# Kernel tuning notes

Hardware: AMD Instinct MI355X
Metric: run time of the kernel (lower is better)

The kernel has to match this reference:

```python
import jax, jax.numpy as jnp
import numpy as np
from jax import lax


def _maxpool_nchw(x, k):
    # Non-overlapping kxk max pool over the last two dims (NCHW).
    return lax.reduce_window(x, -jnp.inf, lax.max,
                             window_dimensions=(1, 1, k, k),
                             window_strides=(1, 1, k, k),
                             padding='VALID')


def setup_inputs() -> dict:
    key = jax.random.key(0)
    k1, k2, k3, k4, k5 = jax.random.split(key, 5)
    B = 16
    return {
        'input_tensor1': jax.random.normal(k1, (B, 128, 48, 48), jnp.float32),
        'input_tensor2': jax.random.normal(k2, (B, 64, 96, 96), jnp.float32),
        'input_tensor3': jax.random.normal(k3, (B, 32, 192, 192), jnp.float32),
        'input_tensor4': jax.random.normal(k4, (B, 16, 384, 384), jnp.float32),
        'pure_ff': jax.random.normal(k5, (B, 256, 24, 24), jnp.float32),
    }


def reference(input_tensor1, input_tensor2, input_tensor3, input_tensor4, pure_ff):
    # and then max-pools. Pooling is per-channel, so this equals pooling once
    # and tiling the pooled result along the channel axis -- same math,
    # without materializing the redundant concat intermediates.
    x1 = jnp.tile(_maxpool_nchw(input_tensor1, 2), (1, 2, 1, 1))   # [B,256,24,24]
    x2 = jnp.tile(_maxpool_nchw(input_tensor2, 4), (1, 4, 1, 1))   # [B,256,24,24]
    x3 = jnp.tile(_maxpool_nchw(input_tensor3, 8), (1, 8, 1, 1))   # [B,256,24,24]
    x4 = jnp.tile(_maxpool_nchw(input_tensor4, 16), (1, 16, 1, 1)) # [B,256,24,24]
    return jax.nn.relu(x1 + x2 + x3 + x4 + pure_ff)
```

## Files before the change

kernel.cpp:

```cpp
#include <hip/hip_runtime.h>
#include <math.h>


namespace {

constexpr int OHW = 24;

__device__ __forceinline__ float fmax4(const float4 v) {
  return fmaxf(fmaxf(v.x, v.y), fmaxf(v.z, v.w));
}

__global__ __launch_bounds__(256, 3) void fused_block(const float* __restrict__ x1,
                                                      const float* __restrict__ x2,
                                                      const float* __restrict__ x3,
                                                      const float* __restrict__ x4,
                                                      const float* __restrict__ ff,
                                                      float* __restrict__ out) {
  __shared__ __attribute__((aligned(16))) float s1[128 * 12];
  __shared__ __attribute__((aligned(16))) float s2[64 * 12];
  __shared__ __attribute__((aligned(16))) float s3[32 * 12];
  __shared__ __attribute__((aligned(16))) float s4[16 * 12];

  const int blk  = blockIdx.x;
  const int b    = blk / 48;
  const int rem  = blk % 48;
  const int oh   = rem >> 1;
  const int half = rem & 1;
  const int tid  = threadIdx.x;

  {
    const float* base = x1 + (size_t)b * 128 * 2304 + oh * 2 * 48 + half * 24;
#pragma unroll
    for (int it = 0; it < 3; ++it) {
      const int t  = it * 256 + tid;
      const int ch = t / 6, pid = t % 6;
      const float* p = base + (size_t)ch * 2304 + pid * 4;
      const float4 a = *reinterpret_cast<const float4*>(p);
      const float4 c = *reinterpret_cast<const float4*>(p + 48);
      s1[ch * 12 + pid * 2]     = fmaxf(fmaxf(a.x, a.y), fmaxf(c.x, c.y));
      s1[ch * 12 + pid * 2 + 1] = fmaxf(fmaxf(a.z, a.w), fmaxf(c.z, c.w));
    }
  }

  {
    const float* base = x2 + (size_t)b * 64 * 9216 + oh * 4 * 96 + half * 48;
#pragma unroll
    for (int it = 0; it < 3; ++it) {
      const int t  = it * 256 + tid;
      const int ch = t / 12, ow = t % 12;
      const float* p = base + (size_t)ch * 9216 + ow * 4;
      float m = -INFINITY;
#pragma unroll
      for (int r = 0; r < 4; ++r)
        m = fmaxf(m, fmax4(*reinterpret_cast<const float4*>(p + r * 96)));
      s2[ch * 12 + ow] = m;
    }
  }

  {
    const float* base = x3 + (size_t)b * 32 * 36864 + oh * 8 * 192 + half * 96;
#pragma unroll
    for (int it = 0; it < 3; ++it) {
      const int t  = it * 256 + tid;
      const int ch = t / 24, ow = (t % 24) >> 1, hf = t & 1;
      const float* p = base + (size_t)ch * 36864 + ow * 8 + hf * 4;
      float m = -INFINITY;
#pragma unroll
      for (int r = 0; r < 8; ++r)
        m = fmaxf(m, fmax4(*reinterpret_cast<const float4*>(p + r * 192)));
      m = fmaxf(m, __shfl_xor(m, 1));
      if (hf == 0) s3[ch * 12 + ow] = m;
    }
  }

  {
    const float* base = x4 + (size_t)b * 16 * 147456 + oh * 16 * 384 + half * 192;
#pragma unroll
    for (int it = 0; it < 3; ++it) {
      const int t  = it * 256 + tid;
      const int ch = t / 48, ow = (t % 48) >> 2, q = t & 3;
      const float* p = base + (size_t)ch * 147456 + ow * 16 + q * 4;
      float m = -INFINITY;
#pragma unroll
      for (int r = 0; r < 16; ++r)
        m = fmaxf(m, fmax4(*reinterpret_cast<const float4*>(p + r * 384)));
      m = fmaxf(m, __shfl_xor(m, 1));
      m = fmaxf(m, __shfl_xor(m, 2));
      if (q == 0) s4[ch * 12 + ow] = m;
    }
  }

  __syncthreads();

  {
    const size_t obase = (size_t)b * 256 * 576 + oh * OHW + half * 12;
#pragma unroll
    for (int it = 0; it < 3; ++it) {
      const int t = it * 256 + tid;
      const int c = t / 3, q = (t % 3) * 4;
      const float4 a1 = *reinterpret_cast<const float4*>(&s1[(c & 127) * 12 + q]);
      const float4 a2 = *reinterpret_cast<const float4*>(&s2[(c & 63)  * 12 + q]);
      const float4 a3 = *reinterpret_cast<const float4*>(&s3[(c & 31)  * 12 + q]);
      const float4 a4 = *reinterpret_cast<const float4*>(&s4[(c & 15)  * 12 + q]);
      const size_t o  = obase + (size_t)c * 576 + q;
      const float4 f  = *reinterpret_cast<const float4*>(ff + o);
      float4 r;
      r.x = fmaxf((((a1.x + a2.x) + a3.x) + a4.x) + f.x, 0.0f);
      r.y = fmaxf((((a1.y + a2.y) + a3.y) + a4.y) + f.y, 0.0f);
      r.z = fmaxf((((a1.z + a2.z) + a3.z) + a4.z) + f.z, 0.0f);
      r.w = fmaxf((((a1.w + a2.w) + a3.w) + a4.w) + f.w, 0.0f);
      *reinterpret_cast<float4*>(out + o) = r;
    }
  }
}

}

extern "C" void kernel_launch(void* const* d_in, const int* in_sizes, int n_in,
                              void* d_out, int out_size, void* d_ws, size_t ws_size,
                              hipStream_t stream) {
  const float* x1 = (const float*)d_in[0];
  const float* x2 = (const float*)d_in[1];
  const float* x3 = (const float*)d_in[2];
  const float* x4 = (const float*)d_in[3];
  const float* ff = (const float*)d_in[4];
  float* out = (float*)d_out;
  (void)d_ws; (void)ws_size; (void)in_sizes; (void)n_in; (void)out_size;

  fused_block<<<768, 256, 0, stream>>>(x1, x2, x3, x4, ff, out);
}
```

Baseline: 315.0 us.

## Split work into finer blocks of four output columns with transposed shared tiles

Each block now covers one output row and a quarter-width strip of four output columns, giving three times as many blocks (2304), each doing a single pass per input with no inner iteration loop. Loads for each pooling window are issued together into register arrays to raise memory-level parallelism. Launch bounds move to 8 blocks per CU. Shared tiles are transposed to [col][channel] so the epilogue reads them without bank conflicts. The trade-off is shorter contiguous runs per row (32–256 bytes), which may reduce coalescing efficiency, plus more per-block overhead.

Result: no change. 316.2 us (+0.4%).

```diff
diff --git a/kernel.cpp b/kernel.cpp
--- a/kernel.cpp
+++ b/kernel.cpp
@@ -4,113 +4,97 @@
 
 namespace {
 
-constexpr int OHW = 24;
-
 __device__ __forceinline__ float fmax4(const float4 v) {
   return fmaxf(fmaxf(v.x, v.y), fmaxf(v.z, v.w));
 }
 
-__global__ __launch_bounds__(256, 3) void fused_block(const float* __restrict__ x1,
+__global__ __launch_bounds__(256, 8) void fused_block(const float* __restrict__ x1,
                                                       const float* __restrict__ x2,
                                                       const float* __restrict__ x3,
                                                       const float* __restrict__ x4,
                                                       const float* __restrict__ ff,
                                                       float* __restrict__ out) {
-  __shared__ __attribute__((aligned(16))) float s1[128 * 12];
-  __shared__ __attribute__((aligned(16))) float s2[64 * 12];
-  __shared__ __attribute__((aligned(16))) float s3[32 * 12];
-  __shared__ __attribute__((aligned(16))) float s4[16 * 12];
+  __shared__ float s1t[4 * 128];
+  __shared__ float s2t[4 * 64];
+  __shared__ float s3t[4 * 32];
+  __shared__ float s4t[4 * 16];
 
   const int blk  = blockIdx.x;
-  const int b    = blk / 48;
-  const int rem  = blk % 48;
-  const int oh   = rem >> 1;
-  const int half = rem & 1;
+  const int b    = blk / 144;
+  const int rem  = blk % 144;
+  const int oh   = rem / 6;
+  const int quad = rem % 6;
   const int tid  = threadIdx.x;
 
   {
-    const float* base = x1 + (size_t)b * 128 * 2304 + oh * 2 * 48 + half * 24;
-#pragma unroll
-    for (int it = 0; it < 3; ++it) {
-      const int t  = it * 256 + tid;
-      const int ch = t / 6, pid = t % 6;
-      const float* p = base + (size_t)ch * 2304 + pid * 4;
-      const float4 a = *reinterpret_cast<const float4*>(p);
-      const float4 c = *reinterpret_cast<const float4*>(p + 48);
-      s1[ch * 12 + pid * 2]     = fmaxf(fmaxf(a.x, a.y), fmaxf(c.x, c.y));
-      s1[ch * 12 + pid * 2 + 1] = fmaxf(fmaxf(a.z, a.w), fmaxf(c.z, c.w));
-    }
+    const int ch = tid >> 1, pid = tid & 1;
+    const float* p = x1 + (size_t)b * 294912 + (size_t)ch * 2304
+                        + oh * 96 + quad * 8 + pid * 4;
+    const float4 a = *reinterpret_cast<const float4*>(p);
+    const float4 c = *reinterpret_cast<const float4*>(p + 48);
+    s1t[(pid * 2) * 128 + ch]     = fmaxf(fmaxf(a.x, a.y), fmaxf(c.x, c.y));
+    s1t[(pid * 2 + 1) * 128 + ch] = fmaxf(fmaxf(a.z, a.w), fmaxf(c.z, c.w));
   }
 
   {
-    const float* base = x2 + (size_t)b * 64 * 9216 + oh * 4 * 96 + half * 48;
+    const int ch = tid >> 2, ow = tid & 3;
+    const float* p = x2 + (size_t)b * 589824 + (size_t)ch * 9216
+                        + oh * 384 + quad * 16 + ow * 4;
+    float4 v[4];
 #pragma unroll
-    for (int it = 0; it < 3; ++it) {
-      const int t  = it * 256 + tid;
-      const int ch = t / 12, ow = t % 12;
-      const float* p = base + (size_t)ch * 9216 + ow * 4;
-      float m = -INFINITY;
+    for (int r = 0; r < 4; ++r) v[r] = *reinterpret_cast<const float4*>(p + r * 96);
+    float m = fmax4(v[0]);
 #pragma unroll
-      for (int r = 0; r < 4; ++r)
-        m = fmaxf(m, fmax4(*reinterpret_cast<const float4*>(p + r * 96)));
-      s2[ch * 12 + ow] = m;
-    }
+    for (int r = 1; r < 4; ++r) m = fmaxf(m, fmax4(v[r]));
+    s2t[ow * 64 + ch] = m;
   }
 
   {
-    const float* base = x3 + (size_t)b * 32 * 36864 + oh * 8 * 192 + half * 96;
+    const int ch = tid >> 3, ow = (tid >> 1) & 3, hf = tid & 1;
+    const float* p = x3 + (size_t)b * 1179648 + (size_t)ch * 36864
+                        + oh * 1536 + quad * 32 + ow * 8 + hf * 4;
+    float4 v[8];
 #pragma unroll
-    for (int it = 0; it < 3; ++it) {
-      const int t  = it * 256 + tid;
-      const int ch = t / 24, ow = (t % 24) >> 1, hf = t & 1;
-      const float* p = base + (size_t)ch * 36864 + ow * 8 + hf * 4;
-      float m = -INFINITY;
+    for (int r = 0; r < 8; ++r) v[r] = *reinterpret_cast<const float4*>(p + r * 192);
+    float m = fmax4(v[0]);
 #pragma unroll
-      for (int r = 0; r < 8; ++r)
-        m = fmaxf(m, fmax4(*reinterpret_cast<const float4*>(p + r * 192)));
-      m = fmaxf(m, __shfl_xor(m, 1));
-      if (hf == 0) s3[ch * 12 + ow] = m;
-    }
+    for (int r = 1; r < 8; ++r) m = fmaxf(m, fmax4(v[r]));
+    m = fmaxf(m, __shfl_xor(m, 1));
+    if (hf == 0) s3t[ow * 32 + ch] = m;
   }
 
   {
-    const float* base = x4 + (size_t)b * 16 * 147456 + oh * 16 * 384 + half * 192;
+    const int ch = tid >> 4, ow = (tid >> 2) & 3, q = tid & 3;
+    const float* p = x4 + (size_t)b * 2359296 + (size_t)ch * 147456
+                        + oh * 6144 + quad * 64 + ow * 16 + q * 4;
+    float m = -INFINITY;
 #pragma unroll
-    for (int it = 0; it < 3; ++it) {
-      const int t  = it * 256 + tid;
-      const int ch = t / 48, ow = (t % 48) >> 2, q = t & 3;
-      const float* p = base + (size_t)ch * 147456 + ow * 16 + q * 4;
-      float m = -INFINITY;
+    for (int h = 0; h < 2; ++h) {
+      float4 v[8];
 #pragma unroll
-      for (int r = 0; r < 16; ++r)
-        m = fmaxf(m, fmax4(*reinterpret_cast<const float4*>(p + r * 384)));
-      m = fmaxf(m, __shfl_xor(m, 1));
-      m = fmaxf(m, __shfl_xor(m, 2));
-      if (q == 0) s4[ch * 12 + ow] = m;
+      for (int r = 0; r < 8; ++r)
+        v[r] = *reinterpret_cast<const float4*>(p + (h * 8 + r) * 384);
+#pragma unroll
+      for (int r = 0; r < 8; ++r) m = fmaxf(m, fmax4(v[r]));
     }
+    m = fmaxf(m, __shfl_xor(m, 1));
+    m = fmaxf(m, __shfl_xor(m, 2));
+    if (q == 0) s4t[ow * 16 + ch] = m;
   }
 
   __syncthreads();
 
   {
-    const size_t obase = (size_t)b * 256 * 576 + oh * OHW + half * 12;
-#pragma unroll
-    for (int it = 0; it < 3; ++it) {
-      const int t = it * 256 + tid;
-      const int c = t / 3, q = (t % 3) * 4;
-      const float4 a1 = *reinterpret_cast<const float4*>(&s1[(c & 127) * 12 + q]);
-      const float4 a2 = *reinterpret_cast<const float4*>(&s2[(c & 63)  * 12 + q]);
-      const float4 a3 = *reinterpret_cast<const float4*>(&s3[(c & 31)  * 12 + q]);
-      const float4 a4 = *reinterpret_cast<const float4*>(&s4[(c & 15)  * 12 + q]);
-      const size_t o  = obase + (size_t)c * 576 + q;
-      const float4 f  = *reinterpret_cast<const float4*>(ff + o);
-      float4 r;
-      r.x = fmaxf((((a1.x + a2.x) + a3.x) + a4.x) + f.x, 0.0f);
-      r.y = fmaxf((((a1.y + a2.y) + a3.y) + a4.y) + f.y, 0.0f);
-      r.z = fmaxf((((a1.z + a2.z) + a3.z) + a4.z) + f.z, 0.0f);
-      r.w = fmaxf((((a1.w + a2.w) + a3.w) + a4.w) + f.w, 0.0f);
-      *reinterpret_cast<float4*>(out + o) = r;
-    }
+    const int c = tid;
+    const size_t o = (size_t)b * 147456 + (size_t)c * 576 + oh * 24 + quad * 4;
+    const float4 f = *reinterpret_cast<const float4*>(ff + o);
+    const int c1 = c & 127, c2 = c & 63, c3 = c & 31, c4 = c & 15;
+    float4 r;
+    r.x = fmaxf(s1t[0 * 128 + c1] + s2t[0 * 64 + c2] + s3t[0 * 32 + c3] + s4t[0 * 16 + c4] + f.x, 0.0f);
+    r.y = fmaxf(s1t[1 * 128 + c1] + s2t[1 * 64 + c2] + s3t[1 * 32 + c3] + s4t[1 * 16 + c4] + f.y, 0.0f);
+    r.z = fmaxf(s1t[2 * 128 + c1] + s2t[2 * 64 + c2] + s3t[2 * 32 + c3] + s4t[2 * 16 + c4] + f.z, 0.0f);
+    r.w = fmaxf(s1t[3 * 128 + c1] + s2t[3 * 64 + c2] + s3t[3 * 32 + c3] + s4t[3 * 16 + c4] + f.w, 0.0f);
+    *reinterpret_cast<float4*>(out + o) = r;
   }
 }
 
@@ -127,5 +111,5 @@
   float* out = (float*)d_out;
   (void)d_ws; (void)ws_size; (void)in_sizes; (void)n_in; (void)out_size;
 
-  fused_block<<<768, 256, 0, stream>>>(x1, x2, x3, x4, ff, out);
+  fused_block<<<2304, 256, 0, stream>>>(x1, x2, x3, x4, ff, out);
 }
```
